# Optimization experiments

Measured on AMD Instinct MI355X. Metric: run time of the kernel, lower is better.

## Reference

```python
import jax, jax.numpy as jnp
import numpy as np

N = 50000
E = 800000
FEAT, ACT = 96, 32
HID, HEADS = 64, 4
NEG_SLOPE = 0.2


def gat_conv(x, src, dst, W, att_s, att_d, bias):
    # x: [N, F_in]; W: [F_in, H*C]; att_s/att_d: [H, C]; bias: [H*C]
    H, C = att_s.shape
    h = (x @ W).reshape(-1, H, C)                      # [N, H, C]
    a_s = jnp.einsum('nhc,hc->nh', h, att_s)           # [N, H]
    a_d = jnp.einsum('nhc,hc->nh', h, att_d)
    e = jax.nn.leaky_relu(a_s[src] + a_d[dst], NEG_SLOPE)  # [E, H]
    m = jax.ops.segment_max(e, dst, num_segments=N)
    e = jnp.exp(e - m[dst])
    denom = jax.ops.segment_sum(e, dst, num_segments=N)
    alpha = e / (denom[dst] + 1e-16)                   # softmax over incoming edges
    out = jax.ops.segment_sum(alpha[:, :, None] * h[src], dst, num_segments=N)
    return out.reshape(-1, H * C) + bias


def setup_inputs() -> dict:
    key = jax.random.key(0)
    ks = jax.random.split(key, 12)
    node_features = jax.random.normal(ks[0], (N, FEAT), dtype=jnp.float32)
    actions = jax.random.normal(ks[1], (N, ACT), dtype=jnp.float32)
    edge_index = jax.random.randint(ks[2], (2, E), 0, N, dtype=jnp.int64)
    s = 0.1
    return {
        'node_features': node_features,
        'actions': actions,
        'edge_index': edge_index,
        'W_emb': jax.random.normal(ks[3], (FEAT + ACT, HID), dtype=jnp.float32) * s,
        'b_emb': jnp.zeros((HID,), dtype=jnp.float32),
        'W1': jax.random.normal(ks[4], (HID, HEADS * HID), dtype=jnp.float32) * s,
        'att_s1': jax.random.normal(ks[5], (HEADS, HID), dtype=jnp.float32) * s,
        'att_d1': jax.random.normal(ks[6], (HEADS, HID), dtype=jnp.float32) * s,
        'b1': jnp.zeros((HEADS * HID,), dtype=jnp.float32),
        'W2': jax.random.normal(ks[7], (HEADS * HID, HID), dtype=jnp.float32) * s,
        'att_s2': jax.random.normal(ks[8], (1, HID), dtype=jnp.float32) * s,
        'att_d2': jax.random.normal(ks[9], (1, HID), dtype=jnp.float32) * s,
        'b2': jnp.zeros((HID,), dtype=jnp.float32),
        'W_v': jax.random.normal(ks[10], (HID, 1), dtype=jnp.float32) * s,
        'b_v': jnp.zeros((1,), dtype=jnp.float32),
    }


def reference(node_features, actions, edge_index, W_emb, b_emb, W1, att_s1, att_d1, b1,
              W2, att_s2, att_d2, b2, W_v, b_v):
    # add self loops (PyG GATConv default add_self_loops=True)
    loop = jnp.arange(N, dtype=edge_index.dtype)
    src = jnp.concatenate([edge_index[0], loop])
    dst = jnp.concatenate([edge_index[1], loop])
    x = jnp.concatenate([node_features, actions], axis=1)
    x = x @ W_emb + b_emb
    x = jax.nn.relu(gat_conv(x, src, dst, W1, att_s1, att_d1, b1))
    x = jax.nn.relu(gat_conv(x, src, dst, W2, att_s2, att_d2, b2))
    g = jnp.mean(x, axis=0, keepdims=True)  # [1, HID]
    return g @ W_v + b_v                    # [1, 1]
```

## Files before the change

### kernel.cpp

```cpp
#include <hip/hip_runtime.h>
#include <hip/hip_bf16.h>
#include <math.h>

#define FEAT 96
#define ACTF 32

using frag8 = __attribute__((ext_vector_type(8))) short;
using f32x4 = __attribute__((ext_vector_type(4))) float;

__device__ __forceinline__ float lrelu(float x) { return x >= 0.f ? x : 0.2f * x; }
__device__ __forceinline__ void atomAddF(float* p, float v) {
    __hip_atomic_fetch_add(p, v, __ATOMIC_RELAXED, __HIP_MEMORY_SCOPE_AGENT);
}
__device__ __forceinline__ float expc(float x) { return __expf(fminf(x, 60.f)); }
__device__ __forceinline__ unsigned short f2bf(float f) {
    __hip_bfloat16 h = __float2bfloat16(f);
    return *(unsigned short*)&h;
}
__device__ __forceinline__ float bf2f(unsigned short u) {
    return __uint_as_float((unsigned)u << 16);
}
__device__ __forceinline__ float bflo(unsigned u) { return __uint_as_float(u << 16); }
__device__ __forceinline__ float bfhi(unsigned u) { return __uint_as_float(u & 0xffff0000u); }

__global__ __launch_bounds__(256) void xprep(
    const float* __restrict__ nf, const float* __restrict__ act,
    unsigned short* __restrict__ Xh, unsigned short* __restrict__ Xl, long long total) {
    long long i = (long long)blockIdx.x * 256 + threadIdx.x;
    if (i >= total) return;
    int n = (int)(i >> 7), k = (int)(i & 127);
    float v = (k < FEAT) ? nf[(size_t)n * FEAT + k] : act[(size_t)n * ACTF + (k - FEAT)];
    unsigned short h = f2bf(v);
    Xh[i] = h;
    Xl[i] = f2bf(v - bf2f(h));
}

__global__ void w1prep(const float* __restrict__ Wemb, const float* __restrict__ bemb,
                       const float* __restrict__ W1,
                       unsigned short* __restrict__ wfh, unsigned short* __restrict__ wfl,
                       float* __restrict__ bfused) {
    int k = blockIdx.x, c = threadIdx.x;
    if (k < 128) {
        float s = 0.f;
        for (int j = 0; j < 64; ++j) s = fmaf(Wemb[k * 64 + j], W1[j * 256 + c], s);
        unsigned short h = f2bf(s);
        wfh[(size_t)c * 128 + k] = h;
        wfl[(size_t)c * 128 + k] = f2bf(s - bf2f(h));
    } else {
        float s = 0.f;
        for (int j = 0; j < 64; ++j) s = fmaf(bemb[j], W1[j * 256 + c], s);
        bfused[c] = s;
    }
}

__global__ __launch_bounds__(256, 2) void gemm1_mfma_w(
    const unsigned short* __restrict__ Xh, const unsigned short* __restrict__ Xl,
    const unsigned short* __restrict__ wfh, const unsigned short* __restrict__ wfl,
    const float* __restrict__ bfused, const float* __restrict__ att_s,
    const float* __restrict__ att_d, __hip_bfloat16* __restrict__ h1b,
    float* __restrict__ a_s, float* __restrict__ a_d, int N) {
    int w = threadIdx.x >> 6, l = threadIdx.x & 63;
    int r16 = l & 15, kg = l >> 4;
    frag8 bh[4][4], bl[4][4];
    #pragma unroll
    for (int c = 0; c < 4; ++c) {
        int ct = w * 4 + c;
        const short* bhp = (const short*)wfh + (size_t)(ct * 16 + r16) * 128 + kg * 8;
        const short* blp = (const short*)wfl + (size_t)(ct * 16 + r16) * 128 + kg * 8;
        #pragma unroll
        for (int ks = 0; ks < 4; ++ks) {
            bh[c][ks] = *(const frag8*)(bhp + ks * 32);
            bl[c][ks] = *(const frag8*)(blp + ks * 32);
        }
    }
    float biasv[4], awv[4], dwv[4];
    #pragma unroll
    for (int c = 0; c < 4; ++c) {
        int ch = w * 64 + c * 16 + r16;
        biasv[c] = bfused[ch];
        awv[c] = att_s[ch];
        dwv[c] = att_d[ch];
    }
    int ntiles = (N + 15) >> 4;
    for (int tile = blockIdx.x; tile < ntiles; tile += gridDim.x) {
        int nb = tile * 16;
        int arow = nb + r16; if (arow >= N) arow = N - 1;
        const short* ahp = (const short*)Xh + (size_t)arow * 128 + kg * 8;
        const short* alp = (const short*)Xl + (size_t)arow * 128 + kg * 8;
        frag8 ah[4], al[4];
        #pragma unroll
        for (int ks = 0; ks < 4; ++ks) {
            ah[ks] = *(const frag8*)(ahp + ks * 32);
            al[ks] = *(const frag8*)(alp + ks * 32);
        }
        float s_s[4] = {0.f, 0.f, 0.f, 0.f}, s_d[4] = {0.f, 0.f, 0.f, 0.f};
        #pragma unroll
        for (int c = 0; c < 4; ++c) {
            f32x4 acc = (f32x4){0.f, 0.f, 0.f, 0.f};
            #pragma unroll
            for (int ks = 0; ks < 4; ++ks) {
                acc = __builtin_amdgcn_mfma_f32_16x16x32_bf16(ah[ks], bh[c][ks], acc, 0, 0, 0);
                acc = __builtin_amdgcn_mfma_f32_16x16x32_bf16(al[ks], bh[c][ks], acc, 0, 0, 0);
                acc = __builtin_amdgcn_mfma_f32_16x16x32_bf16(ah[ks], bl[c][ks], acc, 0, 0, 0);
            }
            int ch = w * 64 + c * 16 + r16;
            #pragma unroll
            for (int r = 0; r < 4; ++r) {
                int node = nb + kg * 4 + r;
                float v = acc[r] + biasv[c];
                if (node < N) h1b[(size_t)node * 256 + ch] = __float2bfloat16(v);
                s_s[r] = fmaf(v, awv[c], s_s[r]);
                s_d[r] = fmaf(v, dwv[c], s_d[r]);
            }
        }
        #pragma unroll
        for (int r = 0; r < 4; ++r) {
            float vs = s_s[r], vd = s_d[r];
            #pragma unroll
            for (int o = 1; o < 16; o <<= 1) {
                vs += __shfl_xor(vs, o);
                vd += __shfl_xor(vd, o);
            }
            int node = nb + kg * 4 + r;
            if (r16 == 0 && node < N) {
                a_s[(size_t)node * 4 + w] = vs;
                a_d[(size_t)node * 4 + w] = vd;
            }
        }
    }
}

__global__ void w2_prep(const float* __restrict__ W2, __hip_bfloat16* __restrict__ w2t) {
    int i = blockIdx.x * 256 + threadIdx.x;
    int k = i >> 6, c = i & 63;
    w2t[(size_t)c * 256 + k] = __float2bfloat16(W2[i]);
}

__global__ __launch_bounds__(256) void gemm2_mfma(
    const __hip_bfloat16* __restrict__ out1b, const __hip_bfloat16* __restrict__ w2t,
    const float* __restrict__ att_s, const float* __restrict__ att_d,
    __hip_bfloat16* __restrict__ h2b, float* __restrict__ a_s, float* __restrict__ a_d,
    int N) {
    int w = threadIdx.x >> 6, l = threadIdx.x & 63;
    int nb = (blockIdx.x * 4 + w) * 16;
    if (nb >= N) return;
    int r16 = l & 15, kg = l >> 4;
    const short* A = (const short*)out1b;
    int arow = min(nb + r16, N - 1);
    const short* arp = A + (size_t)arow * 256 + kg * 8;
    frag8 a[8];
    #pragma unroll
    for (int ks = 0; ks < 8; ++ks) a[ks] = *(const frag8*)(arp + ks * 32);
    const short* B = (const short*)w2t;
    f32x4 acc[4];
    #pragma unroll
    for (int ct = 0; ct < 4; ++ct) {
        acc[ct] = (f32x4){0.f, 0.f, 0.f, 0.f};
        const short* brp = B + (size_t)(ct * 16 + r16) * 256 + kg * 8;
        #pragma unroll
        for (int ks = 0; ks < 8; ++ks) {
            frag8 b = *(const frag8*)(brp + ks * 32);
            acc[ct] = __builtin_amdgcn_mfma_f32_16x16x32_bf16(a[ks], b, acc[ct], 0, 0, 0);
        }
    }
    float s_s[4] = {0.f, 0.f, 0.f, 0.f}, s_d[4] = {0.f, 0.f, 0.f, 0.f};
    #pragma unroll
    for (int ct = 0; ct < 4; ++ct) {
        int ch = ct * 16 + r16;
        float aw = att_s[ch], dw = att_d[ch];
        #pragma unroll
        for (int r = 0; r < 4; ++r) {
            int node = nb + kg * 4 + r;
            float v = acc[ct][r];
            if (node < N) h2b[(size_t)node * 64 + ch] = __float2bfloat16(v);
            s_s[r] = fmaf(v, aw, s_s[r]);
            s_d[r] = fmaf(v, dw, s_d[r]);
        }
    }
    #pragma unroll
    for (int r = 0; r < 4; ++r) {
        #pragma unroll
        for (int o = 1; o < 16; o <<= 1) {
            s_s[r] += __shfl_xor(s_s[r], o);
            s_d[r] += __shfl_xor(s_d[r], o);
        }
        int node = nb + kg * 4 + r;
        if (r16 == 0 && node < N) { a_s[node] = s_s[r]; a_d[node] = s_d[r]; }
    }
}

__global__ void hist_kernel(const int* __restrict__ dst, int* __restrict__ cnt, int E, int ET) {
    int e = blockIdx.x * blockDim.x + threadIdx.x;
    if (e >= ET) return;
    int d = (e < E) ? dst[e] : (e - E);
    atomicAdd(&cnt[d], 1);
}

__global__ __launch_bounds__(256) void scan_blocks(
    const int* __restrict__ cnt, int* __restrict__ off, int* __restrict__ bsum, int n) {
    int b = blockIdx.x, t = threadIdx.x;
    int i = b * 256 + t;
    int v = (i < n) ? cnt[i] : 0;
    int lane = t & 63, w = t >> 6;
    int x = v;
    #pragma unroll
    for (int o = 1; o < 64; o <<= 1) {
        int y = __shfl_up(x, o);
        if (lane >= o) x += y;
    }
    __shared__ int wtot[4];
    if (lane == 63) wtot[w] = x;
    __syncthreads();
    int add = 0;
    #pragma unroll
    for (int j = 0; j < 4; ++j) if (j < w) add += wtot[j];
    int incl = x + add;
    if (i < n) off[i] = incl - v;
    if (t == 255) bsum[b] = incl;
}

__global__ __launch_bounds__(256) void scan_tops(
    const int* __restrict__ bsum, int* __restrict__ bpre, int nb) {
    int t = threadIdx.x;
    int v = (t < nb) ? bsum[t] : 0;
    int lane = t & 63, w = t >> 6;
    int x = v;
    #pragma unroll
    for (int o = 1; o < 64; o <<= 1) {
        int y = __shfl_up(x, o);
        if (lane >= o) x += y;
    }
    __shared__ int wtot[4];
    if (lane == 63) wtot[w] = x;
    __syncthreads();
    int add = 0;
    #pragma unroll
    for (int j = 0; j < 4; ++j) if (j < w) add += wtot[j];
    if (t < nb) bpre[t] = x + add - v;
    if (t == 255) bpre[nb] = x + add;
}

__global__ __launch_bounds__(256) void scan_add(
    const int* __restrict__ bpre, int* __restrict__ off, int n, int nb) {
    int b = blockIdx.x, t = threadIdx.x;
    int i = b * 256 + t;
    if (i < n) off[i] += bpre[b];
    if (b == 0 && t == 0) off[n] = bpre[nb];
}

__global__ void scatter_kernel(const int* __restrict__ src, const int* __restrict__ dst,
                               const int* __restrict__ off, int* __restrict__ cur,
                               int* __restrict__ perm, int E, int ET) {
    int e = blockIdx.x * blockDim.x + threadIdx.x;
    if (e >= ET) return;
    int s = (e < E) ? src[e] : (e - E);
    int d = (e < E) ? dst[e] : (e - E);
    int r = atomicAdd(&cur[d], 1);
    perm[off[d] + r] = s;
}

__global__ __launch_bounds__(256) void fused_gat4(
    const int* __restrict__ off, const int* __restrict__ perm,
    const float* __restrict__ a_s, const float* __restrict__ a_d,
    const __hip_bfloat16* __restrict__ h1b, const float* __restrict__ bias,
    __hip_bfloat16* __restrict__ out1b, int N) {
    __shared__ float exls[4][64][4];
    __shared__ unsigned idxls[4][64];
    int w = threadIdx.x >> 6, l = threadIdx.x & 63;
    int d = blockIdx.x * 4 + w;
    if (d >= N) return;
    int lo = off[d], hi = off[d + 1];
    const float4* as4 = (const float4*)a_s;
    float4 ad = ((const float4*)a_d)[d];
    float dx = 0.f, dy = 0.f, dz = 0.f, dw = 0.f;
    for (int e = lo + l; e < hi; e += 64) {
        float4 a = as4[perm[e]];
        dx += expc(lrelu(a.x + ad.x));
        dy += expc(lrelu(a.y + ad.y));
        dz += expc(lrelu(a.z + ad.z));
        dw += expc(lrelu(a.w + ad.w));
    }
    #pragma unroll
    for (int o = 32; o; o >>= 1) {
        dx += __shfl_xor(dx, o); dy += __shfl_xor(dy, o);
        dz += __shfl_xor(dz, o); dw += __shfl_xor(dw, o);
    }
    int eg = l >> 5;
    int li = l & 31;
    int gh = li >> 3;
    float rr = 1.f / ((gh == 0 ? dx : gh == 1 ? dy : gh == 2 ? dz : dw) + 1e-16f);
    const char* hb = (const char*)h1b;
    unsigned laneoff = (unsigned)li * 16u;
    float acc[8] = {0.f, 0.f, 0.f, 0.f, 0.f, 0.f, 0.f, 0.f};
    for (int base = lo; base < hi; base += 64) {
        int e = base + l;
        bool valid = e < hi;
        int s = valid ? perm[e] : 0;
        float4 a = as4[s];
        exls[w][l][0] = valid ? expc(lrelu(a.x + ad.x)) : 0.f;
        exls[w][l][1] = valid ? expc(lrelu(a.y + ad.y)) : 0.f;
        exls[w][l][2] = valid ? expc(lrelu(a.z + ad.z)) : 0.f;
        exls[w][l][3] = valid ? expc(lrelu(a.w + ad.w)) : 0.f;
        idxls[w][l] = valid ? (unsigned)s * 512u : 0u;
        int n = min(64, hi - base);
        #pragma unroll 2
        for (int i = 0; i < n; i += 2) {
            int ii = i + eg;
            float ex = exls[w][ii][gh];
            unsigned voff = idxls[w][ii] + laneoff;
            uint4 v = *(const uint4*)(hb + voff);
            acc[0] = fmaf(ex, bflo(v.x), acc[0]);
            acc[1] = fmaf(ex, bfhi(v.x), acc[1]);
            acc[2] = fmaf(ex, bflo(v.y), acc[2]);
            acc[3] = fmaf(ex, bfhi(v.y), acc[3]);
            acc[4] = fmaf(ex, bflo(v.z), acc[4]);
            acc[5] = fmaf(ex, bfhi(v.z), acc[5]);
            acc[6] = fmaf(ex, bflo(v.w), acc[6]);
            acc[7] = fmaf(ex, bfhi(v.w), acc[7]);
        }
    }
    #pragma unroll
    for (int j = 0; j < 8; ++j) acc[j] += __shfl_xor(acc[j], 32);
    if (eg == 0) {
        float4 b0 = ((const float4*)bias)[li * 2];
        float4 b1 = ((const float4*)bias)[li * 2 + 1];
        uint4 pk;
        pk.x = (unsigned)f2bf(fmaxf(fmaf(acc[0], rr, b0.x), 0.f))
             | ((unsigned)f2bf(fmaxf(fmaf(acc[1], rr, b0.y), 0.f)) << 16);
        pk.y = (unsigned)f2bf(fmaxf(fmaf(acc[2], rr, b0.z), 0.f))
             | ((unsigned)f2bf(fmaxf(fmaf(acc[3], rr, b0.w), 0.f)) << 16);
        pk.z = (unsigned)f2bf(fmaxf(fmaf(acc[4], rr, b1.x), 0.f))
             | ((unsigned)f2bf(fmaxf(fmaf(acc[5], rr, b1.y), 0.f)) << 16);
        pk.w = (unsigned)f2bf(fmaxf(fmaf(acc[6], rr, b1.z), 0.f))
             | ((unsigned)f2bf(fmaxf(fmaf(acc[7], rr, b1.w), 0.f)) << 16);
        ((uint4*)(out1b + (size_t)d * 256))[li] = pk;
    }
}

__global__ __launch_bounds__(256) void fused_gat1(
    const int* __restrict__ off, const int* __restrict__ perm,
    const float* __restrict__ a_s, const float* __restrict__ a_d,
    const __hip_bfloat16* __restrict__ h2b, const float* __restrict__ bias,
    float* __restrict__ out2, int N) {
    __shared__ float exls1[4][64];
    __shared__ unsigned idxls1[4][64];
    int w = threadIdx.x >> 6, l = threadIdx.x & 63;
    int d = blockIdx.x * 4 + w;
    if (d >= N) return;
    int lo = off[d], hi = off[d + 1];
    float add = a_d[d];
    float den = 0.f;
    for (int e = lo + l; e < hi; e += 64)
        den += expc(lrelu(a_s[perm[e]] + add));
    #pragma unroll
    for (int o = 32; o; o >>= 1) den += __shfl_xor(den, o);
    float rr = 1.f / (den + 1e-16f);
    int eg = l >> 4;
    int li = l & 15;
    const char* hb = (const char*)h2b;
    unsigned laneoff = (unsigned)li * 8u;
    float acc0 = 0.f, acc1 = 0.f, acc2 = 0.f, acc3 = 0.f;
    for (int base = lo; base < hi; base += 64) {
        int e = base + l;
        bool valid = e < hi;
        int s = valid ? perm[e] : 0;
        exls1[w][l] = valid ? expc(lrelu(a_s[s] + add)) : 0.f;
        idxls1[w][l] = valid ? (unsigned)s * 128u : 0u;
        int n = min(64, hi - base);
        #pragma unroll 4
        for (int i = 0; i < n; i += 4) {
            int ii = i + eg;
            float ex = exls1[w][ii];
            unsigned voff = idxls1[w][ii] + laneoff;
            uint2 v = *(const uint2*)(hb + voff);
            acc0 = fmaf(ex, bflo(v.x), acc0);
            acc1 = fmaf(ex, bfhi(v.x), acc1);
            acc2 = fmaf(ex, bflo(v.y), acc2);
            acc3 = fmaf(ex, bfhi(v.y), acc3);
        }
    }
    #pragma unroll
    for (int o = 16; o < 64; o <<= 1) {
        acc0 += __shfl_xor(acc0, o);
        acc1 += __shfl_xor(acc1, o);
        acc2 += __shfl_xor(acc2, o);
        acc3 += __shfl_xor(acc3, o);
    }
    if (eg == 0 && (l >> 4) == 0) {
        const float4* b4 = (const float4*)bias;
        float4 bv = b4[li];
        float4 o4;
        o4.x = fmaxf(fmaf(acc0, rr, bv.x), 0.f);
        o4.y = fmaxf(fmaf(acc1, rr, bv.y), 0.f);
        o4.z = fmaxf(fmaf(acc2, rr, bv.z), 0.f);
        o4.w = fmaxf(fmaf(acc3, rr, bv.w), 0.f);
        ((float4*)(out2 + (size_t)d * 64))[li] = o4;
    }
}

__global__ void colsum_kernel(const float* __restrict__ x, float* __restrict__ g, int N) {
    __shared__ float part[4][64];
    int c = threadIdx.x & 63;
    int r = threadIdx.x >> 6;
    float acc = 0.f;
    for (long long n = (long long)blockIdx.x * 4 + r; n < N; n += (long long)gridDim.x * 4)
        acc += x[n * 64 + c];
    part[r][c] = acc;
    __syncthreads();
    if (r == 0) {
        float v = part[0][c] + part[1][c] + part[2][c] + part[3][c];
        atomAddF(&g[c], v);
    }
}

__global__ void final_kernel(const float* __restrict__ g, const float* __restrict__ Wv,
                             const float* __restrict__ bv, float* __restrict__ out, int N) {
    int lane = threadIdx.x;
    float v = (g[lane] / (float)N) * Wv[lane];
    #pragma unroll
    for (int off = 32; off; off >>= 1) v += __shfl_down(v, off);
    if (lane == 0) out[0] = v + bv[0];
}

extern "C" void kernel_launch(void* const* d_in, const int* in_sizes, int n_in,
                              void* d_out, int out_size, void* d_ws, size_t ws_size,
                              hipStream_t stream) {
    const float* nf   = (const float*)d_in[0];
    const float* act  = (const float*)d_in[1];
    const int*   ei   = (const int*)d_in[2];
    const float* Wemb = (const float*)d_in[3];
    const float* bemb = (const float*)d_in[4];
    const float* W1   = (const float*)d_in[5];
    const float* as1  = (const float*)d_in[6];
    const float* ad1  = (const float*)d_in[7];
    const float* b1   = (const float*)d_in[8];
    const float* W2   = (const float*)d_in[9];
    const float* as2  = (const float*)d_in[10];
    const float* ad2  = (const float*)d_in[11];
    const float* b2   = (const float*)d_in[12];
    const float* Wv   = (const float*)d_in[13];
    const float* bv   = (const float*)d_in[14];
    float* out = (float*)d_out;

    const int N = in_sizes[0] / FEAT;
    const int E = in_sizes[2] / 2;
    const int ET = E + N;
    const int* srcp = ei;
    const int* dstp = ei + E;
    const int NB = (N + 255) / 256;

    char* ws = (char*)d_ws;
    unsigned short* Xh = (unsigned short*)ws;
    unsigned short* Xl = Xh + (size_t)N * 128;
    __hip_bfloat16* h1b   = (__hip_bfloat16*)(Xl + (size_t)N * 128);
    __hip_bfloat16* out1b = h1b + (size_t)N * 256;
    float* a_s  = (float*)(out1b + (size_t)N * 256);
    float* a_d  = a_s + (size_t)N * 4;
    __hip_bfloat16* h2b = (__hip_bfloat16*)(a_d + (size_t)N * 4);
    float* out2 = (float*)(h2b + (size_t)N * 64);
    float* g    = out2 + (size_t)N * 64;
    __hip_bfloat16* w2t = (__hip_bfloat16*)(g + 64);
    unsigned short* wfh = (unsigned short*)(w2t + 64 * 256);
    unsigned short* wfl = wfh + 256 * 128;
    float* bfused = (float*)(wfl + 256 * 128);
    int* cnt  = (int*)Xh;
    int* off  = cnt + N;
    int* cur  = off + N + 1;
    int* perm = cur + N;
    int* bsum = perm + ET;
    int* bpre = bsum + NB;

    (void)ws_size; (void)n_in; (void)out_size;

    long long xtot = (long long)N * 128;
    xprep<<<(int)((xtot + 255) / 256), 256, 0, stream>>>(nf, act, Xh, Xl, xtot);
    w1prep<<<129, 256, 0, stream>>>(Wemb, bemb, W1, wfh, wfl, bfused);
    w2_prep<<<64, 256, 0, stream>>>(W2, w2t);

    gemm1_mfma_w<<<1024, 256, 0, stream>>>(Xh, Xl, wfh, wfl, bfused,
                                           as1, ad1, h1b, a_s, a_d, N);

    hipMemsetAsync(cnt, 0, (size_t)N * sizeof(int), stream);
    hipMemsetAsync(cur, 0, (size_t)N * sizeof(int), stream);
    hist_kernel<<<(ET + 255) / 256, 256, 0, stream>>>(dstp, cnt, E, ET);
    scan_blocks<<<NB, 256, 0, stream>>>(cnt, off, bsum, N);
    scan_tops<<<1, 256, 0, stream>>>(bsum, bpre, NB);
    scan_add<<<NB, 256, 0, stream>>>(bpre, off, N, NB);
    scatter_kernel<<<(ET + 255) / 256, 256, 0, stream>>>(srcp, dstp, off, cur, perm, E, ET);

    fused_gat4<<<(N + 3) / 4, 256, 0, stream>>>(off, perm, a_s, a_d, h1b, b1, out1b, N);

    gemm2_mfma<<<(N + 63) / 64, 256, 0, stream>>>(out1b, w2t, as2, ad2, h2b, a_s, a_d, N);
    fused_gat1<<<(N + 3) / 4, 256, 0, stream>>>(off, perm, a_s, a_d, h2b, b2, out2, N);

    hipMemsetAsync(g, 0, 64 * sizeof(float), stream);
    colsum_kernel<<<512, 256, 0, stream>>>(out2, g, N);
    final_kernel<<<1, 64, 0, stream>>>(g, Wv, bv, out, N);
}
```

Measured before the change: 297.6 us.

## Merge prep kernels, fuse colsum with final reduction, persist gemm2 weights

Folds the three weight and input prep kernels into one launch, and merges the two memsets into one by reordering the cnt and cur buffers. It folds the g/done zeroing into scan_tops and fuses the final dot product into colsum using a last-block atomic counter. gemm2 becomes a persistent grid-stride kernel that keeps the W2 fragments in registers across tiles. The aim is to cut launch count and repeated weight loads, at the cost of more register pressure in gemm2 and an extra atomic fence per colsum block.

```diff
diff --git a/kernel.cpp b/kernel.cpp
--- a/kernel.cpp
+++ b/kernel.cpp
@@ -23,34 +23,47 @@
 __device__ __forceinline__ float bflo(unsigned u) { return __uint_as_float(u << 16); }
 __device__ __forceinline__ float bfhi(unsigned u) { return __uint_as_float(u & 0xffff0000u); }
 
-__global__ __launch_bounds__(256) void xprep(
+__global__ __launch_bounds__(256) void prep_all(
     const float* __restrict__ nf, const float* __restrict__ act,
-    unsigned short* __restrict__ Xh, unsigned short* __restrict__ Xl, long long total) {
-    long long i = (long long)blockIdx.x * 256 + threadIdx.x;
-    if (i >= total) return;
-    int n = (int)(i >> 7), k = (int)(i & 127);
-    float v = (k < FEAT) ? nf[(size_t)n * FEAT + k] : act[(size_t)n * ACTF + (k - FEAT)];
-    unsigned short h = f2bf(v);
-    Xh[i] = h;
-    Xl[i] = f2bf(v - bf2f(h));
-}
-
-__global__ void w1prep(const float* __restrict__ Wemb, const float* __restrict__ bemb,
-                       const float* __restrict__ W1,
-                       unsigned short* __restrict__ wfh, unsigned short* __restrict__ wfl,
-                       float* __restrict__ bfused) {
-    int k = blockIdx.x, c = threadIdx.x;
-    if (k < 128) {
-        float s = 0.f;
-        for (int j = 0; j < 64; ++j) s = fmaf(Wemb[k * 64 + j], W1[j * 256 + c], s);
-        unsigned short h = f2bf(s);
-        wfh[(size_t)c * 128 + k] = h;
-        wfl[(size_t)c * 128 + k] = f2bf(s - bf2f(h));
-    } else {
-        float s = 0.f;
-        for (int j = 0; j < 64; ++j) s = fmaf(bemb[j], W1[j * 256 + c], s);
-        bfused[c] = s;
-    }
+    unsigned short* __restrict__ Xh, unsigned short* __restrict__ Xl,
+    long long xtot, int xb,
+    const float* __restrict__ Wemb, const float* __restrict__ bemb,
+    const float* __restrict__ W1,
+    unsigned short* __restrict__ wfh, unsigned short* __restrict__ wfl,
+    float* __restrict__ bfused,
+    const float* __restrict__ W2, __hip_bfloat16* __restrict__ w2t) {
+    int b = blockIdx.x;
+    if (b < xb) {
+        long long i = (long long)b * 256 + threadIdx.x;
+        if (i < xtot) {
+            int n = (int)(i >> 7), k = (int)(i & 127);
+            float v = (k < FEAT) ? nf[(size_t)n * FEAT + k] : act[(size_t)n * ACTF + (k - FEAT)];
+            unsigned short h = f2bf(v);
+            Xh[i] = h;
+            Xl[i] = f2bf(v - bf2f(h));
+        }
+        return;
+    }
+    b -= xb;
+    if (b < 129) {
+        int k = b, c = threadIdx.x;
+        if (k < 128) {
+            float s = 0.f;
+            for (int j = 0; j < 64; ++j) s = fmaf(Wemb[k * 64 + j], W1[j * 256 + c], s);
+            unsigned short h = f2bf(s);
+            wfh[(size_t)c * 128 + k] = h;
+            wfl[(size_t)c * 128 + k] = f2bf(s - bf2f(h));
+        } else {
+            float s = 0.f;
+            for (int j = 0; j < 64; ++j) s = fmaf(bemb[j], W1[j * 256 + c], s);
+            bfused[c] = s;
+        }
+        return;
+    }
+    b -= 129;
+    int i = b * 256 + threadIdx.x;
+    int k = i >> 6, c = i & 63;
+    w2t[(size_t)c * 256 + k] = __float2bfloat16(W2[i]);
 }
 
 __global__ __launch_bounds__(256, 2) void gemm1_mfma_w(
@@ -130,62 +143,65 @@
     }
 }
 
-__global__ void w2_prep(const float* __restrict__ W2, __hip_bfloat16* __restrict__ w2t) {
-    int i = blockIdx.x * 256 + threadIdx.x;
-    int k = i >> 6, c = i & 63;
-    w2t[(size_t)c * 256 + k] = __float2bfloat16(W2[i]);
-}
-
-__global__ __launch_bounds__(256) void gemm2_mfma(
+__global__ __launch_bounds__(256, 2) void gemm2_mfma_w(
     const __hip_bfloat16* __restrict__ out1b, const __hip_bfloat16* __restrict__ w2t,
     const float* __restrict__ att_s, const float* __restrict__ att_d,
     __hip_bfloat16* __restrict__ h2b, float* __restrict__ a_s, float* __restrict__ a_d,
     int N) {
     int w = threadIdx.x >> 6, l = threadIdx.x & 63;
-    int nb = (blockIdx.x * 4 + w) * 16;
-    if (nb >= N) return;
     int r16 = l & 15, kg = l >> 4;
-    const short* A = (const short*)out1b;
-    int arow = min(nb + r16, N - 1);
-    const short* arp = A + (size_t)arow * 256 + kg * 8;
-    frag8 a[8];
-    #pragma unroll
-    for (int ks = 0; ks < 8; ++ks) a[ks] = *(const frag8*)(arp + ks * 32);
     const short* B = (const short*)w2t;
-    f32x4 acc[4];
+    frag8 b[4][8];
     #pragma unroll
     for (int ct = 0; ct < 4; ++ct) {
-        acc[ct] = (f32x4){0.f, 0.f, 0.f, 0.f};
         const short* brp = B + (size_t)(ct * 16 + r16) * 256 + kg * 8;
         #pragma unroll
-        for (int ks = 0; ks < 8; ++ks) {
-            frag8 b = *(const frag8*)(brp + ks * 32);
-            acc[ct] = __builtin_amdgcn_mfma_f32_16x16x32_bf16(a[ks], b, acc[ct], 0, 0, 0);
-        }
-    }
-    float s_s[4] = {0.f, 0.f, 0.f, 0.f}, s_d[4] = {0.f, 0.f, 0.f, 0.f};
+        for (int ks = 0; ks < 8; ++ks)
+            b[ct][ks] = *(const frag8*)(brp + ks * 32);
+    }
+    float awv[4], dwv[4];
     #pragma unroll
     for (int ct = 0; ct < 4; ++ct) {
         int ch = ct * 16 + r16;
-        float aw = att_s[ch], dw = att_d[ch];
+        awv[ct] = att_s[ch];
+        dwv[ct] = att_d[ch];
+    }
+    const short* A = (const short*)out1b;
+    int ntiles = (N + 15) >> 4;
+    for (int tile = blockIdx.x * 4 + w; tile < ntiles; tile += gridDim.x * 4) {
+        int nb = tile * 16;
+        int arow = nb + r16; if (arow >= N) arow = N - 1;
+        const short* arp = A + (size_t)arow * 256 + kg * 8;
+        frag8 a[8];
+        #pragma unroll
+        for (int ks = 0; ks < 8; ++ks) a[ks] = *(const frag8*)(arp + ks * 32);
+        float s_s[4] = {0.f, 0.f, 0.f, 0.f}, s_d[4] = {0.f, 0.f, 0.f, 0.f};
+        #pragma unroll
+        for (int ct = 0; ct < 4; ++ct) {
+            f32x4 acc = (f32x4){0.f, 0.f, 0.f, 0.f};
+            #pragma unroll
+            for (int ks = 0; ks < 8; ++ks)
+                acc = __builtin_amdgcn_mfma_f32_16x16x32_bf16(a[ks], b[ct][ks], acc, 0, 0, 0);
+            int ch = ct * 16 + r16;
+            #pragma unroll
+            for (int r = 0; r < 4; ++r) {
+                int node = nb + kg * 4 + r;
+                float v = acc[r];
+                if (node < N) h2b[(size_t)node * 64 + ch] = __float2bfloat16(v);
+                s_s[r] = fmaf(v, awv[ct], s_s[r]);
+                s_d[r] = fmaf(v, dwv[ct], s_d[r]);
+            }
+        }
         #pragma unroll
         for (int r = 0; r < 4; ++r) {
+            #pragma unroll
+            for (int o = 1; o < 16; o <<= 1) {
+                s_s[r] += __shfl_xor(s_s[r], o);
+                s_d[r] += __shfl_xor(s_d[r], o);
+            }
             int node = nb + kg * 4 + r;
-            float v = acc[ct][r];
-            if (node < N) h2b[(size_t)node * 64 + ch] = __float2bfloat16(v);
-            s_s[r] = fmaf(v, aw, s_s[r]);
-            s_d[r] = fmaf(v, dw, s_d[r]);
-        }
-    }
-    #pragma unroll
-    for (int r = 0; r < 4; ++r) {
-        #pragma unroll
-        for (int o = 1; o < 16; o <<= 1) {
-            s_s[r] += __shfl_xor(s_s[r], o);
-            s_d[r] += __shfl_xor(s_d[r], o);
-        }
-        int node = nb + kg * 4 + r;
-        if (r16 == 0 && node < N) { a_s[node] = s_s[r]; a_d[node] = s_d[r]; }
+            if (r16 == 0 && node < N) { a_s[node] = s_s[r]; a_d[node] = s_d[r]; }
+        }
     }
 }
 
@@ -220,7 +236,8 @@
 }
 
 __global__ __launch_bounds__(256) void scan_tops(
-    const int* __restrict__ bsum, int* __restrict__ bpre, int nb) {
+    const int* __restrict__ bsum, int* __restrict__ bpre, int nb,
+    float* __restrict__ g, int* __restrict__ done) {
     int t = threadIdx.x;
     int v = (t < nb) ? bsum[t] : 0;
     int lane = t & 63, w = t >> 6;
@@ -238,6 +255,8 @@
     for (int j = 0; j < 4; ++j) if (j < w) add += wtot[j];
     if (t < nb) bpre[t] = x + add - v;
     if (t == 255) bpre[nb] = x + add;
+    if (t < 64) g[t] = 0.f;
+    if (t == 64) *done = 0;
 }
 
 __global__ __launch_bounds__(256) void scan_add(
@@ -398,8 +417,12 @@
     }
 }
 
-__global__ void colsum_kernel(const float* __restrict__ x, float* __restrict__ g, int N) {
+__global__ __launch_bounds__(256) void colsum_final(
+    const float* __restrict__ x, float* __restrict__ g, int* __restrict__ done,
+    const float* __restrict__ Wv, const float* __restrict__ bv,
+    float* __restrict__ out, int N) {
     __shared__ float part[4][64];
+    __shared__ int amlast;
     int c = threadIdx.x & 63;
     int r = threadIdx.x >> 6;
     float acc = 0.f;
@@ -411,15 +434,19 @@
         float v = part[0][c] + part[1][c] + part[2][c] + part[3][c];
         atomAddF(&g[c], v);
     }
-}
-
-__global__ void final_kernel(const float* __restrict__ g, const float* __restrict__ Wv,
-                             const float* __restrict__ bv, float* __restrict__ out, int N) {
-    int lane = threadIdx.x;
-    float v = (g[lane] / (float)N) * Wv[lane];
-    #pragma unroll
-    for (int off = 32; off; off >>= 1) v += __shfl_down(v, off);
-    if (lane == 0) out[0] = v + bv[0];
+    __threadfence();
+    if (threadIdx.x == 0) {
+        int t = __hip_atomic_fetch_add(done, 1, __ATOMIC_ACQ_REL, __HIP_MEMORY_SCOPE_AGENT);
+        amlast = (t == (int)gridDim.x - 1) ? 1 : 0;
+    }
+    __syncthreads();
+    if (amlast && threadIdx.x < 64) {
+        float gc = __hip_atomic_load(&g[threadIdx.x], __ATOMIC_RELAXED, __HIP_MEMORY_SCOPE_AGENT);
+        float v = (gc / (float)N) * Wv[threadIdx.x];
+        #pragma unroll
+        for (int o = 32; o; o >>= 1) v += __shfl_down(v, o);
+        if (threadIdx.x == 0) out[0] = v + bv[0];
+    }
 }
 
 extern "C" void kernel_launch(void* const* d_in, const int* in_sizes, int n_in,
@@ -464,36 +491,35 @@
     unsigned short* wfl = wfh + 256 * 128;
     float* bfused = (float*)(wfl + 256 * 128);
     int* cnt  = (int*)Xh;
-    int* off  = cnt + N;
-    int* cur  = off + N + 1;
-    int* perm = cur + N;
+    int* cur  = cnt + N;
+    int* off  = cur + N;
+    int* perm = off + N + 1;
     int* bsum = perm + ET;
     int* bpre = bsum + NB;
+    int* done = bpre + NB + 1;
 
     (void)ws_size; (void)n_in; (void)out_size;
 
     long long xtot = (long long)N * 128;
-    xprep<<<(int)((xtot + 255) / 256), 256, 0, stream>>>(nf, act, Xh, Xl, xtot);
-    w1prep<<<129, 256, 0, stream>>>(Wemb, bemb, W1, wfh, wfl, bfused);
-    w2_prep<<<64, 256, 0, stream>>>(W2, w2t);
+    const int XB = (int)((xtot + 255) / 256);
+    prep_all<<<XB + 129 + 64, 256, 0, stream>>>(nf, act, Xh, Xl, xtot, XB,
+                                                Wemb, bemb, W1, wfh, wfl, bfused,
+                                                W2, w2t);
 
     gemm1_mfma_w<<<1024, 256, 0, stream>>>(Xh, Xl, wfh, wfl, bfused,
                                            as1, ad1, h1b, a_s, a_d, N);
 
-    hipMemsetAsync(cnt, 0, (size_t)N * sizeof(int), stream);
-    hipMemsetAsync(cur, 0, (size_t)N * sizeof(int), stream);
+    hipMemsetAsync(cnt, 0, (size_t)2 * N * sizeof(int), stream);
     hist_kernel<<<(ET + 255) / 256, 256, 0, stream>>>(dstp, cnt, E, ET);
     scan_blocks<<<NB, 256, 0, stream>>>(cnt, off, bsum, N);
-    scan_tops<<<1, 256, 0, stream>>>(bsum, bpre, NB);
+    scan_tops<<<1, 256, 0, stream>>>(bsum, bpre, NB, g, done);
     scan_add<<<NB, 256, 0, stream>>>(bpre, off, N, NB);
     scatter_kernel<<<(ET + 255) / 256, 256, 0, stream>>>(srcp, dstp, off, cur, perm, E, ET);
 
     fused_gat4<<<(N + 3) / 4, 256, 0, stream>>>(off, perm, a_s, a_d, h1b, b1, out1b, N);
 
-    gemm2_mfma<<<(N + 63) / 64, 256, 0, stream>>>(out1b, w2t, as2, ad2, h2b, a_s, a_d, N);
+    gemm2_mfma_w<<<512, 256, 0, stream>>>(out1b, w2t, as2, ad2, h2b, a_s, a_d, N);
     fused_gat1<<<(N + 3) / 4, 256, 0, stream>>>(off, perm, a_s, a_d, h2b, b2, out2, N);
 
-    hipMemsetAsync(g, 0, 64 * sizeof(float), stream);
-    colsum_kernel<<<512, 256, 0, stream>>>(out2, g, N);
-    final_kernel<<<1, 64, 0, stream>>>(g, Wv, bv, out, N);
-}
+    colsum_final<<<512, 256, 0, stream>>>(out2, g, done, Wv, bv, out, N);
+}
```

After: 298.3 us. Within noise of the previous version (+0.2%).
